# Performance work log

Measured on AMD Instinct MI355X. Metric: run time of the kernel, lower is better.

The kernel has to match this reference:

```python
import jax, jax.numpy as jnp
import numpy as np

NUM_CLUSTERS = 8
DIM_IN, DIM_HID = 1024, 256
N = 65536


def setup_inputs() -> dict:
    key = jax.random.key(0)
    ks = jax.random.split(key, 12)
    s_in = 1.0 / np.sqrt(DIM_IN)
    s_h = 1.0 / np.sqrt(DIM_HID)
    return {
        "x_path": jax.random.normal(ks[0], (1, N, DIM_IN), dtype=jnp.float32),
        "cluster_id": jax.random.randint(ks[1], (N,), 0, NUM_CLUSTERS),
        "W1": jax.random.normal(ks[2], (DIM_HID, DIM_IN), dtype=jnp.float32) * s_in,
        "b1": jax.random.normal(ks[3], (DIM_HID,), dtype=jnp.float32) * s_in,
        "Wf": jax.random.normal(ks[4], (DIM_HID, DIM_HID), dtype=jnp.float32) * s_h,
        "bf": jax.random.normal(ks[5], (DIM_HID,), dtype=jnp.float32) * s_h,
        "Wa": jax.random.normal(ks[6], (DIM_HID, DIM_HID), dtype=jnp.float32) * s_h,
        "ba": jax.random.normal(ks[7], (DIM_HID,), dtype=jnp.float32) * s_h,
        "Wb": jax.random.normal(ks[8], (DIM_HID, DIM_HID), dtype=jnp.float32) * s_h,
        "bb": jax.random.normal(ks[9], (DIM_HID,), dtype=jnp.float32) * s_h,
        "Wc": jax.random.normal(ks[10], (1, DIM_HID), dtype=jnp.float32) * s_h,
        "bc": jax.random.normal(ks[11], (1,), dtype=jnp.float32) * s_h,
    }


def reference(x_path, cluster_id, W1, b1, Wf, bf, Wa, ba, Wb, bb, Wc, bc):
    x = x_path[0]  # [N, dim_in]
    # per-instance 1x1 conv + ReLU (== linear + ReLU)
    h = jax.nn.relu(jnp.einsum('nd,hd->nh', x, W1) + b1)  # [N, dim_hid]
    # segment mean over clusters (AdaptiveAvgPool1d(1) per cluster); empty -> 0
    seg_sum = jax.ops.segment_sum(h, cluster_id, num_segments=NUM_CLUSTERS)
    counts = jax.ops.segment_sum(jnp.ones((h.shape[0],), h.dtype), cluster_id,
                                 num_segments=NUM_CLUSTERS)
    h_cluster = seg_sum / jnp.maximum(counts, 1.0)[:, None]  # [K, dim_hid]
    # attention net: Linear + ReLU (dropout is inference identity)
    h_path = jax.nn.relu(h_cluster @ Wf.T + bf)  # [K, dim_hid]
    # gated attention (CLAM Attn_Net_Gated)
    a = jnp.tanh(h_path @ Wa.T + ba)
    g = jax.nn.sigmoid(h_path @ Wb.T + bb)
    A = (a * g) @ Wc.T + bc            # [K, 1]
    A = jax.nn.softmax(A.T, axis=1)    # [1, K]
    H = A @ h_path                     # [1, dim_hid]
    return H
```

## Files before the change

kernel.cpp:

```cpp
#include <hip/hip_runtime.h>
#include <hip/hip_bf16.h>

#define NN    65536
#define KDIM  1024
#define HDIM  256
#define NC    8
#define BM    64
#define NSP   8

typedef __bf16 bf16x8 __attribute__((ext_vector_type(8)));
typedef float  f32x4  __attribute__((ext_vector_type(4)));
typedef __attribute__((address_space(1))) void GV;
typedef __attribute__((address_space(3))) void LV;

static __device__ __forceinline__ void async_cp16(const void* g, void* l) {
    __builtin_amdgcn_global_load_lds((GV*)g, (LV*)l, 16, 0, 0);
}

#define WAIT_VM16()  __builtin_amdgcn_s_waitcnt(0x4F70)
#define SCHED_PIN()  __builtin_amdgcn_sched_barrier(0)

static __device__ __forceinline__ unsigned short f2bf_rne(float f) {
    unsigned int u = __float_as_uint(f);
    unsigned int r = u + 0x7fffu + ((u >> 16) & 1u);
    return (unsigned short)(r >> 16);
}

static __device__ __forceinline__ unsigned long long pack4bf(float4 v) {
    return (unsigned long long)f2bf_rne(v.x)
         | ((unsigned long long)f2bf_rne(v.y) << 16)
         | ((unsigned long long)f2bf_rne(v.z) << 32)
         | ((unsigned long long)f2bf_rne(v.w) << 48);
}

static __device__ __forceinline__ bf16x8 cvt8(f32x4 a, f32x4 b) {
    __hip_bfloat162 p0 = __float22bfloat162_rn(float2{a[0], a[1]});
    __hip_bfloat162 p1 = __float22bfloat162_rn(float2{a[2], a[3]});
    __hip_bfloat162 p2 = __float22bfloat162_rn(float2{b[0], b[1]});
    __hip_bfloat162 p3 = __float22bfloat162_rn(float2{b[2], b[3]});
    union { __hip_bfloat162 h[4]; bf16x8 v; } u;
    u.h[0] = p0; u.h[1] = p1; u.h[2] = p2; u.h[3] = p3;
    return u.v;
}

__global__ __launch_bounds__(256) void prep_kernel(
    const float* __restrict__ W1, unsigned short* __restrict__ W1b,
    const int* __restrict__ cid, int* __restrict__ cnt_partial)
{
    __shared__ int hcnt[NC];
    if (threadIdx.x < NC) hcnt[threadIdx.x] = 0;
    __syncthreads();

    const int gid  = blockIdx.x * 256 + threadIdx.x;
    const int lane = gid & 63;
    const int j    = (gid >> 6) & 3;
    const int wv   = (gid >> 8) & 3;
    const int kb   = gid >> 10;
    const int n    = wv * 64 + j * 16 + (lane & 15);
    const int k0   = kb * 32 + (lane >> 4) * 8;
    const float* src = W1 + (size_t)n * KDIM + k0;
    float4 v0 = *(const float4*)(src);
    float4 v1 = *(const float4*)(src + 4);
    ulonglong2 pk;
    pk.x = pack4bf(v0);
    pk.y = pack4bf(v1);
    *(ulonglong2*)(W1b + (size_t)gid * 8) = pk;

    atomicAdd(&hcnt[cid[gid]], 1);
    atomicAdd(&hcnt[cid[gid + 32768]], 1);
    __syncthreads();
    if (threadIdx.x < NC)
        cnt_partial[blockIdx.x * NC + threadIdx.x] = hcnt[threadIdx.x];
}

__global__ __launch_bounds__(256, 2) void gemm_kernel(
    const float* __restrict__ x, const int* __restrict__ cid,
    const unsigned short* __restrict__ W1b, const float* __restrict__ b1,
    float* __restrict__ partial)
{
    __shared__ __align__(16) char xs[2 * 32768];
    float* lsums = (float*)xs;
    int*   cids  = (int*)(xs + 8192);

    const int tid  = threadIdx.x;
    const int wave = tid >> 6;
    const int lane = tid & 63;
    const int l15  = lane & 15;
    const int q    = lane >> 4;
    const int row0 = blockIdx.x * BM;
    const int rot  = blockIdx.x & 7;

    int myc = 0;
    if (tid < BM) myc = cid[row0 + tid];

    const int lrow  = lane >> 5;
    const int lslot = lane & 31;

    const int le0 = l15 * 512 + (((2 * q + 0) ^ (l15 & 7)) << 4);
    const int le1 = l15 * 512 + (((2 * q + 1) ^ (l15 & 7)) << 4);

    const unsigned short* bg = W1b + (size_t)(wave * 256 + lane) * 8;

    f32x4 acc[4][4];
    #pragma unroll
    for (int i = 0; i < 4; ++i)
        #pragma unroll
        for (int j = 0; j < 4; ++j)
            #pragma unroll
            for (int r = 0; r < 4; ++r) acc[i][j][r] = 0.0f;

    bf16x8 bA[16], bB[16];

    {
        const int pp0 = rot;
        #pragma unroll
        for (int t = 0; t < 8; ++t) {
            const int r7 = (2 * t + lrow) & 7;
            const float* src = x + (size_t)(row0 + wave * 16 + 2 * t + lrow) * KDIM
                             + pp0 * 128 + ((lslot ^ r7) << 2);
            async_cp16(src, &xs[(wave * 8 + t) * 1024]);
        }
        SCHED_PIN();
        #pragma unroll
        for (int ks = 0; ks < 4; ++ks)
            #pragma unroll
            for (int j = 0; j < 4; ++j)
                bA[ks * 4 + j] = *(const bf16x8*)(bg + (size_t)(pp0 * 4 + ks) * 8192 + j * 512);
        SCHED_PIN();
        WAIT_VM16();
        __builtin_amdgcn_s_barrier();
        SCHED_PIN();
    }

    #pragma unroll
    for (int p = 0; p < NSP; ++p) {
        const int buf = p & 1;
        bf16x8* curB = (p & 1) ? bB : bA;
        bf16x8* nxtB = (p & 1) ? bA : bB;

        if (p + 1 < NSP) {
            const int pp1 = (p + 1 + rot) & 7;
            #pragma unroll
            for (int t = 0; t < 8; ++t) {
                const int r7 = (2 * t + lrow) & 7;
                const float* src = x + (size_t)(row0 + wave * 16 + 2 * t + lrow) * KDIM
                                 + pp1 * 128 + ((lslot ^ r7) << 2);
                async_cp16(src, &xs[(1 - buf) * 32768 + (wave * 8 + t) * 1024]);
            }
            SCHED_PIN();
            #pragma unroll
            for (int ks = 0; ks < 4; ++ks)
                #pragma unroll
                for (int j = 0; j < 4; ++j)
                    nxtB[ks * 4 + j] = *(const bf16x8*)(bg + (size_t)(pp1 * 4 + ks) * 8192 + j * 512);
        }

        #pragma unroll
        for (int ks = 0; ks < 4; ++ks) {
            bf16x8 af[4];
            #pragma unroll
            for (int i = 0; i < 4; ++i) {
                const f32x4 v0 = *(const f32x4*)&xs[buf * 32768 + i * 8192 + ks * 128 + le0];
                const f32x4 v1 = *(const f32x4*)&xs[buf * 32768 + i * 8192 + ks * 128 + le1];
                af[i] = cvt8(v0, v1);
            }
            #pragma unroll
            for (int i = 0; i < 4; ++i)
                #pragma unroll
                for (int j = 0; j < 4; ++j)
                    acc[i][j] = __builtin_amdgcn_mfma_f32_16x16x32_bf16(af[i], curB[ks * 4 + j], acc[i][j], 0, 0, 0);
        }

        if (p + 1 < NSP) {
            SCHED_PIN();
            WAIT_VM16();
            __builtin_amdgcn_s_barrier();
            SCHED_PIN();
        }
    }

    {
        const f32x4 z = {0.0f, 0.0f, 0.0f, 0.0f};
        *(f32x4*)&lsums[tid * 8]     = z;
        *(f32x4*)&lsums[tid * 8 + 4] = z;
        if (tid < BM) cids[tid] = myc;
    }
    __syncthreads();

    float b1v[4];
    #pragma unroll
    for (int j = 0; j < 4; ++j) b1v[j] = b1[wave * 64 + j * 16 + l15];

    #pragma unroll
    for (int i = 0; i < 4; ++i) {
        #pragma unroll
        for (int j = 0; j < 4; ++j) {
            const int col = wave * 64 + j * 16 + l15;
            #pragma unroll
            for (int r = 0; r < 4; ++r) {
                float v = fmaxf(acc[i][j][r] + b1v[j], 0.0f);
                int m = i * 16 + q * 4 + r;
                atomicAdd(&lsums[col * NC + cids[m]], v);
            }
        }
    }
    __syncthreads();
    float* dst = partial + (size_t)blockIdx.x * 2048 + tid * 8;
    *(f32x4*)dst       = *(const f32x4*)&lsums[tid * 8];
    *(f32x4*)(dst + 4) = *(const f32x4*)&lsums[tid * 8 + 4];
}

__global__ __launch_bounds__(256) void reduce_kernel(
    const float* __restrict__ partial, float* __restrict__ stage2)
{
    const int s  = blockIdx.x >> 3;
    const int og = blockIdx.x & 7;
    const int o  = og * 256 + threadIdx.x;
    const float* p = partial + (size_t)s * 128 * 2048 + o;
    float a0=0,a1=0,a2=0,a3=0,a4=0,a5=0,a6=0,a7=0;
    #pragma unroll 4
    for (int pb = 0; pb < 128; pb += 8) {
        a0 += p[(size_t)(pb+0)*2048]; a1 += p[(size_t)(pb+1)*2048];
        a2 += p[(size_t)(pb+2)*2048]; a3 += p[(size_t)(pb+3)*2048];
        a4 += p[(size_t)(pb+4)*2048]; a5 += p[(size_t)(pb+5)*2048];
        a6 += p[(size_t)(pb+6)*2048]; a7 += p[(size_t)(pb+7)*2048];
    }
    stage2[(size_t)s * 2048 + o] = ((a0+a1)+(a2+a3)) + ((a4+a5)+(a6+a7));
}

__global__ __launch_bounds__(256) void head_kernel(
    const float* __restrict__ stage2, const int* __restrict__ cnt_partial,
    const float* __restrict__ Wf, const float* __restrict__ bf1,
    const float* __restrict__ Wa, const float* __restrict__ ba,
    const float* __restrict__ Wb, const float* __restrict__ bb,
    const float* __restrict__ Wc, const float* __restrict__ bc,
    float* __restrict__ out)
{
    __shared__ float hcT[HDIM * NC];
    __shared__ float hpT[HDIM * NC];
    __shared__ float red[NC * 4];
    __shared__ int   cnt_s[256];
    __shared__ float cnt_f[NC];
    const int c = threadIdx.x;
    const int wave = c >> 6, lane = c & 63;

    {
        int k = c & 7, g = c >> 3;
        const int* cp = cnt_partial + g * 32 + k;
        cnt_s[c] = cp[0] + cp[8] + cp[16] + cp[24];
    }
    __syncthreads();
    if (c < NC) {
        int s = 0;
        #pragma unroll
        for (int g = 0; g < 32; ++g) s += cnt_s[g * 8 + c];
        cnt_f[c] = 1.0f / fmaxf((float)s, 1.0f);
    }
    __syncthreads();

    {
        float a[NC] = {0,0,0,0,0,0,0,0};
        #pragma unroll
        for (int s = 0; s < 8; ++s) {
            f32x4 u0 = *(const f32x4*)&stage2[(size_t)s * 2048 + c * 8];
            f32x4 u1 = *(const f32x4*)&stage2[(size_t)s * 2048 + c * 8 + 4];
            a[0]+=u0[0]; a[1]+=u0[1]; a[2]+=u0[2]; a[3]+=u0[3];
            a[4]+=u1[0]; a[5]+=u1[1]; a[6]+=u1[2]; a[7]+=u1[3];
        }
        #pragma unroll
        for (int k = 0; k < NC; ++k) hcT[c * NC + k] = a[k] * cnt_f[k];
    }
    __syncthreads();

    {
        float acc[NC];
        float bias = bf1[c];
        #pragma unroll
        for (int k = 0; k < NC; ++k) acc[k] = bias;
        const float4* wf4 = (const float4*)(Wf + (size_t)c * HDIM);
        for (int d4 = 0; d4 < 64; ++d4) {
            float4 w = wf4[d4];
            #pragma unroll
            for (int e = 0; e < 4; ++e) {
                float wd = (e == 0) ? w.x : (e == 1) ? w.y : (e == 2) ? w.z : w.w;
                const f32x4 h0 = *(const f32x4*)&hcT[(d4 * 4 + e) * NC];
                const f32x4 h1 = *(const f32x4*)&hcT[(d4 * 4 + e) * NC + 4];
                acc[0] += wd * h0[0]; acc[1] += wd * h0[1];
                acc[2] += wd * h0[2]; acc[3] += wd * h0[3];
                acc[4] += wd * h1[0]; acc[5] += wd * h1[1];
                acc[6] += wd * h1[2]; acc[7] += wd * h1[3];
            }
        }
        #pragma unroll
        for (int k = 0; k < NC; ++k) hpT[c * NC + k] = fmaxf(acc[k], 0.0f);
    }
    __syncthreads();

    float za[NC], zb[NC];
    {
        float biasa = ba[c], biasb = bb[c];
        #pragma unroll
        for (int k = 0; k < NC; ++k) { za[k] = biasa; zb[k] = biasb; }
        const float4* wa4 = (const float4*)(Wa + (size_t)c * HDIM);
        const float4* wb4 = (const float4*)(Wb + (size_t)c * HDIM);
        for (int d4 = 0; d4 < 64; ++d4) {
            float4 wa = wa4[d4], wb = wb4[d4];
            #pragma unroll
            for (int e = 0; e < 4; ++e) {
                float wav = (e == 0) ? wa.x : (e == 1) ? wa.y : (e == 2) ? wa.z : wa.w;
                float wbv = (e == 0) ? wb.x : (e == 1) ? wb.y : (e == 2) ? wb.z : wb.w;
                const f32x4 h0 = *(const f32x4*)&hpT[(d4 * 4 + e) * NC];
                const f32x4 h1 = *(const f32x4*)&hpT[(d4 * 4 + e) * NC + 4];
                za[0] += wav * h0[0]; za[1] += wav * h0[1]; za[2] += wav * h0[2]; za[3] += wav * h0[3];
                za[4] += wav * h1[0]; za[5] += wav * h1[1]; za[6] += wav * h1[2]; za[7] += wav * h1[3];
                zb[0] += wbv * h0[0]; zb[1] += wbv * h0[1]; zb[2] += wbv * h0[2]; zb[3] += wbv * h0[3];
                zb[4] += wbv * h1[0]; zb[5] += wbv * h1[1]; zb[6] += wbv * h1[2]; zb[7] += wbv * h1[3];
            }
        }
    }
    float wcv = Wc[c];
    float v[NC];
    #pragma unroll
    for (int k = 0; k < NC; ++k) {
        float a = tanhf(za[k]);
        float g = 1.0f / (1.0f + expf(-zb[k]));
        v[k] = a * g * wcv;
    }
    #pragma unroll
    for (int k = 0; k < NC; ++k) {
        float s = v[k];
        #pragma unroll
        for (int off = 32; off > 0; off >>= 1) s += __shfl_down(s, off, 64);
        if (lane == 0) red[k * 4 + wave] = s;
    }
    __syncthreads();
    float logit[NC], m = -1e30f;
    #pragma unroll
    for (int k = 0; k < NC; ++k) {
        logit[k] = red[k * 4] + red[k * 4 + 1] + red[k * 4 + 2] + red[k * 4 + 3] + bc[0];
        m = fmaxf(m, logit[k]);
    }
    float s = 0.0f, ex[NC];
    #pragma unroll
    for (int k = 0; k < NC; ++k) { ex[k] = expf(logit[k] - m); s += ex[k]; }
    float inv = 1.0f / s;
    float o = 0.0f;
    #pragma unroll
    for (int k = 0; k < NC; ++k) o += ex[k] * inv * hpT[c * NC + k];
    out[c] = o;
}

extern "C" void kernel_launch(void* const* d_in, const int* in_sizes, int n_in,
                              void* d_out, int out_size, void* d_ws, size_t ws_size,
                              hipStream_t stream)
{
    (void)in_sizes; (void)n_in; (void)out_size; (void)ws_size;
    const float* x   = (const float*)d_in[0];
    const int*   cid = (const int*)  d_in[1];
    const float* W1  = (const float*)d_in[2];
    const float* b1  = (const float*)d_in[3];
    const float* Wf  = (const float*)d_in[4];
    const float* bfv = (const float*)d_in[5];
    const float* Wa  = (const float*)d_in[6];
    const float* ba  = (const float*)d_in[7];
    const float* Wb  = (const float*)d_in[8];
    const float* bb  = (const float*)d_in[9];
    const float* Wc  = (const float*)d_in[10];
    const float* bc  = (const float*)d_in[11];
    float* out = (float*)d_out;

    unsigned short* W1b   = (unsigned short*)d_ws;
    int*   cnt_partial    = (int*)  ((char*)d_ws + 524288);
    float* partial        = (float*)((char*)d_ws + 528384);
    float* stage2         = (float*)((char*)d_ws + 528384 + 8388608);

    hipLaunchKernelGGL(prep_kernel,   dim3(128),     dim3(256), 0, stream, W1, W1b, cid, cnt_partial);
    hipLaunchKernelGGL(gemm_kernel,   dim3(NN / BM), dim3(256), 0, stream, x, cid, W1b, b1, partial);
    hipLaunchKernelGGL(reduce_kernel, dim3(64),      dim3(256), 0, stream, partial, stage2);
    hipLaunchKernelGGL(head_kernel,   dim3(1),       dim3(256), 0, stream,
                       stage2, cnt_partial, Wf, bfv, Wa, ba, Wb, bb, Wc, bc, out);
}
```

Measured before the change: 500.1 us.

## Convert x tile to bf16 before staging in LDS, two K-halves

Replaces the double-buffered async global→LDS fp32 pipeline with register loads of x that are converted to bf16 and written to LDS, covering half of K (512) per phase. The MFMA loop then reads bf16 fragments straight from LDS and prefetches B two k-steps ahead. This halves LDS footprint and traffic per element and removes the per-fragment conversion from the inner loop. In exchange, the async copy overlap is lost: each half loads and converts fully before compute, with two barriers per half and no overlap between x loading and MFMA work.

```diff
diff --git a/kernel.cpp b/kernel.cpp
--- a/kernel.cpp
+++ b/kernel.cpp
@@ -6,19 +6,9 @@
 #define HDIM  256
 #define NC    8
 #define BM    64
-#define NSP   8
 
 typedef __bf16 bf16x8 __attribute__((ext_vector_type(8)));
 typedef float  f32x4  __attribute__((ext_vector_type(4)));
-typedef __attribute__((address_space(1))) void GV;
-typedef __attribute__((address_space(3))) void LV;
-
-static __device__ __forceinline__ void async_cp16(const void* g, void* l) {
-    __builtin_amdgcn_global_load_lds((GV*)g, (LV*)l, 16, 0, 0);
-}
-
-#define WAIT_VM16()  __builtin_amdgcn_s_waitcnt(0x4F70)
-#define SCHED_PIN()  __builtin_amdgcn_sched_barrier(0)
 
 static __device__ __forceinline__ unsigned short f2bf_rne(float f) {
     unsigned int u = __float_as_uint(f);
@@ -33,14 +23,12 @@
          | ((unsigned long long)f2bf_rne(v.w) << 48);
 }
 
-static __device__ __forceinline__ bf16x8 cvt8(f32x4 a, f32x4 b) {
-    __hip_bfloat162 p0 = __float22bfloat162_rn(float2{a[0], a[1]});
-    __hip_bfloat162 p1 = __float22bfloat162_rn(float2{a[2], a[3]});
-    __hip_bfloat162 p2 = __float22bfloat162_rn(float2{b[0], b[1]});
-    __hip_bfloat162 p3 = __float22bfloat162_rn(float2{b[2], b[3]});
-    union { __hip_bfloat162 h[4]; bf16x8 v; } u;
-    u.h[0] = p0; u.h[1] = p1; u.h[2] = p2; u.h[3] = p3;
-    return u.v;
+static __device__ __forceinline__ uint2 cvt4_u(float4 v) {
+    union { __hip_bfloat162 h; unsigned int u; } a, b;
+    a.h = __float22bfloat162_rn(float2{v.x, v.y});
+    b.h = __float22bfloat162_rn(float2{v.z, v.w});
+    uint2 r; r.x = a.u; r.y = b.u;
+    return r;
 }
 
 __global__ __launch_bounds__(256) void prep_kernel(
@@ -78,7 +66,7 @@
     const unsigned short* __restrict__ W1b, const float* __restrict__ b1,
     float* __restrict__ partial)
 {
-    __shared__ __align__(16) char xs[2 * 32768];
+    __shared__ __align__(16) char xs[65536];
     float* lsums = (float*)xs;
     int*   cids  = (int*)(xs + 8192);
 
@@ -88,17 +76,10 @@
     const int l15  = lane & 15;
     const int q    = lane >> 4;
     const int row0 = blockIdx.x * BM;
-    const int rot  = blockIdx.x & 7;
 
     int myc = 0;
     if (tid < BM) myc = cid[row0 + tid];
 
-    const int lrow  = lane >> 5;
-    const int lslot = lane & 31;
-
-    const int le0 = l15 * 512 + (((2 * q + 0) ^ (l15 & 7)) << 4);
-    const int le1 = l15 * 512 + (((2 * q + 1) ^ (l15 & 7)) << 4);
-
     const unsigned short* bg = W1b + (size_t)(wave * 256 + lane) * 8;
 
     f32x4 acc[4][4];
@@ -109,74 +90,69 @@
             #pragma unroll
             for (int r = 0; r < 4; ++r) acc[i][j][r] = 0.0f;
 
-    bf16x8 bA[16], bB[16];
-
-    {
-        const int pp0 = rot;
-        #pragma unroll
-        for (int t = 0; t < 8; ++t) {
-            const int r7 = (2 * t + lrow) & 7;
-            const float* src = x + (size_t)(row0 + wave * 16 + 2 * t + lrow) * KDIM
-                             + pp0 * 128 + ((lslot ^ r7) << 2);
-            async_cp16(src, &xs[(wave * 8 + t) * 1024]);
-        }
-        SCHED_PIN();
-        #pragma unroll
-        for (int ks = 0; ks < 4; ++ks)
-            #pragma unroll
-            for (int j = 0; j < 4; ++j)
-                bA[ks * 4 + j] = *(const bf16x8*)(bg + (size_t)(pp0 * 4 + ks) * 8192 + j * 512);
-        SCHED_PIN();
-        WAIT_VM16();
-        __builtin_amdgcn_s_barrier();
-        SCHED_PIN();
-    }
-
-    #pragma unroll
-    for (int p = 0; p < NSP; ++p) {
-        const int buf = p & 1;
-        bf16x8* curB = (p & 1) ? bB : bA;
-        bf16x8* nxtB = (p & 1) ? bA : bB;
-
-        if (p + 1 < NSP) {
-            const int pp1 = (p + 1 + rot) & 7;
+    #pragma unroll
+    for (int kh = 0; kh < 2; ++kh) {
+        {
+            const float* base = x + (size_t)(row0 + wave * 16) * KDIM + kh * 512 + lane * 4;
+            float4 v[2][8];
             #pragma unroll
             for (int t = 0; t < 8; ++t) {
-                const int r7 = (2 * t + lrow) & 7;
-                const float* src = x + (size_t)(row0 + wave * 16 + 2 * t + lrow) * KDIM
-                                 + pp1 * 128 + ((lslot ^ r7) << 2);
-                async_cp16(src, &xs[(1 - buf) * 32768 + (wave * 8 + t) * 1024]);
-            }
-            SCHED_PIN();
-            #pragma unroll
-            for (int ks = 0; ks < 4; ++ks)
+                const int r = t >> 1, c = t & 1;
+                v[0][t] = *(const float4*)(base + (size_t)r * KDIM + c * 256);
+            }
+            #pragma unroll
+            for (int b = 0; b < 4; ++b) {
+                if (b + 1 < 4) {
+                    #pragma unroll
+                    for (int t = 0; t < 8; ++t) {
+                        const int tt = (b + 1) * 8 + t, r = tt >> 1, c = tt & 1;
+                        v[(b + 1) & 1][t] = *(const float4*)(base + (size_t)r * KDIM + c * 256);
+                    }
+                }
                 #pragma unroll
-                for (int j = 0; j < 4; ++j)
-                    nxtB[ks * 4 + j] = *(const bf16x8*)(bg + (size_t)(pp1 * 4 + ks) * 8192 + j * 512);
-        }
-
-        #pragma unroll
-        for (int ks = 0; ks < 4; ++ks) {
-            bf16x8 af[4];
-            #pragma unroll
-            for (int i = 0; i < 4; ++i) {
-                const f32x4 v0 = *(const f32x4*)&xs[buf * 32768 + i * 8192 + ks * 128 + le0];
-                const f32x4 v1 = *(const f32x4*)&xs[buf * 32768 + i * 8192 + ks * 128 + le1];
-                af[i] = cvt8(v0, v1);
-            }
-            #pragma unroll
-            for (int i = 0; i < 4; ++i)
+                for (int t = 0; t < 8; ++t) {
+                    const int tt = b * 8 + t, r = tt >> 1, c = tt & 1;
+                    const int rl = wave * 16 + r;
+                    const int s  = c * 32 + (lane >> 1);
+                    const int h  = lane & 1;
+                    uint2 pk = cvt4_u(v[b & 1][t]);
+                    *(uint2*)&xs[rl * 1024 + (((s ^ (rl & 7)) << 4) | (h << 3))] = pk;
+                }
+            }
+        }
+        __syncthreads();
+
+        {
+            const unsigned short* bgh = bg + (size_t)kh * 16 * 8192;
+            bf16x8 Bf[2][4];
+            #pragma unroll
+            for (int j = 0; j < 4; ++j) Bf[0][j] = *(const bf16x8*)(bgh + j * 512);
+            #pragma unroll
+            for (int j = 0; j < 4; ++j) Bf[1][j] = *(const bf16x8*)(bgh + 8192 + j * 512);
+
+            #pragma unroll
+            for (int kb = 0; kb < 16; ++kb) {
+                const int p = kb & 1;
+                bf16x8 a4[4];
                 #pragma unroll
-                for (int j = 0; j < 4; ++j)
-                    acc[i][j] = __builtin_amdgcn_mfma_f32_16x16x32_bf16(af[i], curB[ks * 4 + j], acc[i][j], 0, 0, 0);
-        }
-
-        if (p + 1 < NSP) {
-            SCHED_PIN();
-            WAIT_VM16();
-            __builtin_amdgcn_s_barrier();
-            SCHED_PIN();
-        }
+                for (int i = 0; i < 4; ++i) {
+                    const int rl = i * 16 + l15;
+                    const int s  = kb * 4 + q;
+                    a4[i] = *(const bf16x8*)&xs[rl * 1024 + ((s ^ (rl & 7)) << 4)];
+                }
+                #pragma unroll
+                for (int i = 0; i < 4; ++i)
+                    #pragma unroll
+                    for (int j = 0; j < 4; ++j)
+                        acc[i][j] = __builtin_amdgcn_mfma_f32_16x16x32_bf16(a4[i], Bf[p][j], acc[i][j], 0, 0, 0);
+                if (kb + 2 < 16) {
+                    #pragma unroll
+                    for (int j = 0; j < 4; ++j)
+                        Bf[p][j] = *(const bf16x8*)(bgh + (size_t)(kb + 2) * 8192 + j * 512);
+                }
+            }
+        }
+        __syncthreads();
     }
 
     {
```

New measurement: 538.5 us. +7.7%, slower.

## Split head into three multi-block kernels, widen reduction, remap GEMM block order

Applied to the files above, without the earlier changes.

The single-block head kernel is split into three kernels: an 8-block Wf layer, an 8-block gated-attention layer writing per-block partial logits, and a one-block softmax/output kernel. The goal is to spread the serial head matmuls over more compute units. The reduce stage is widened from 64 to 128 blocks, each summing 64 partials, and GEMM blocks are remapped with a strided pbid so neighbouring blocks touch different row ranges, which changes the memory access pattern. The cost is two extra kernel launches and round trips through global memory.

```diff
diff --git a/kernel.cpp b/kernel.cpp
--- a/kernel.cpp
+++ b/kernel.cpp
@@ -7,6 +7,7 @@
 #define NC    8
 #define BM    64
 #define NSP   8
+#define RSPL  16
 
 typedef __bf16 bf16x8 __attribute__((ext_vector_type(8)));
 typedef float  f32x4  __attribute__((ext_vector_type(4)));
@@ -87,8 +88,9 @@
     const int lane = tid & 63;
     const int l15  = lane & 15;
     const int q    = lane >> 4;
-    const int row0 = blockIdx.x * BM;
-    const int rot  = blockIdx.x & 7;
+    const int pbid = (blockIdx.x & 7) * 128 + (blockIdx.x >> 3);
+    const int row0 = pbid * BM;
+    const int rot  = (blockIdx.x >> 3) & 7;
 
     int myc = 0;
     if (tid < BM) myc = cid[row0 + tid];
@@ -157,18 +159,18 @@
 
         #pragma unroll
         for (int ks = 0; ks < 4; ++ks) {
-            bf16x8 af[4];
+            bf16x8 a4[4];
             #pragma unroll
             for (int i = 0; i < 4; ++i) {
                 const f32x4 v0 = *(const f32x4*)&xs[buf * 32768 + i * 8192 + ks * 128 + le0];
                 const f32x4 v1 = *(const f32x4*)&xs[buf * 32768 + i * 8192 + ks * 128 + le1];
-                af[i] = cvt8(v0, v1);
+                a4[i] = cvt8(v0, v1);
             }
             #pragma unroll
             for (int i = 0; i < 4; ++i)
                 #pragma unroll
                 for (int j = 0; j < 4; ++j)
-                    acc[i][j] = __builtin_amdgcn_mfma_f32_16x16x32_bf16(af[i], curB[ks * 4 + j], acc[i][j], 0, 0, 0);
+                    acc[i][j] = __builtin_amdgcn_mfma_f32_16x16x32_bf16(a4[i], curB[ks * 4 + j], acc[i][j], 0, 0, 0);
         }
 
         if (p + 1 < NSP) {
@@ -205,7 +207,7 @@
         }
     }
     __syncthreads();
-    float* dst = partial + (size_t)blockIdx.x * 2048 + tid * 8;
+    float* dst = partial + (size_t)pbid * 2048 + tid * 8;
     *(f32x4*)dst       = *(const f32x4*)&lsums[tid * 8];
     *(f32x4*)(dst + 4) = *(const f32x4*)&lsums[tid * 8 + 4];
 }
@@ -216,10 +218,10 @@
     const int s  = blockIdx.x >> 3;
     const int og = blockIdx.x & 7;
     const int o  = og * 256 + threadIdx.x;
-    const float* p = partial + (size_t)s * 128 * 2048 + o;
+    const float* p = partial + (size_t)s * 64 * 2048 + o;
     float a0=0,a1=0,a2=0,a3=0,a4=0,a5=0,a6=0,a7=0;
     #pragma unroll 4
-    for (int pb = 0; pb < 128; pb += 8) {
+    for (int pb = 0; pb < 64; pb += 8) {
         a0 += p[(size_t)(pb+0)*2048]; a1 += p[(size_t)(pb+1)*2048];
         a2 += p[(size_t)(pb+2)*2048]; a3 += p[(size_t)(pb+3)*2048];
         a4 += p[(size_t)(pb+4)*2048]; a5 += p[(size_t)(pb+5)*2048];
@@ -228,125 +230,105 @@
     stage2[(size_t)s * 2048 + o] = ((a0+a1)+(a2+a3)) + ((a4+a5)+(a6+a7));
 }
 
-__global__ __launch_bounds__(256) void head_kernel(
+__global__ __launch_bounds__(256) void headA_kernel(
     const float* __restrict__ stage2, const int* __restrict__ cnt_partial,
     const float* __restrict__ Wf, const float* __restrict__ bf1,
+    float* __restrict__ hp_ws)
+{
+    __shared__ float hcT[HDIM * NC];
+    __shared__ int   cnt_s[256];
+    __shared__ float cnt_f[NC];
+    const int t = threadIdx.x;
+
+    {
+        int k = t & 7, g = t >> 3;
+        const int* cp = cnt_partial + g * 32 + k;
+        cnt_s[t] = cp[0] + cp[8] + cp[16] + cp[24];
+    }
+    __syncthreads();
+    if (t < NC) {
+        int s = 0;
+        #pragma unroll
+        for (int g = 0; g < 32; ++g) s += cnt_s[g * 8 + t];
+        cnt_f[t] = 1.0f / fmaxf((float)s, 1.0f);
+    }
+    __syncthreads();
+
+    {
+        float a[NC] = {0,0,0,0,0,0,0,0};
+        #pragma unroll
+        for (int s = 0; s < RSPL; ++s) {
+            f32x4 u0 = *(const f32x4*)&stage2[(size_t)s * 2048 + t * 8];
+            f32x4 u1 = *(const f32x4*)&stage2[(size_t)s * 2048 + t * 8 + 4];
+            a[0]+=u0[0]; a[1]+=u0[1]; a[2]+=u0[2]; a[3]+=u0[3];
+            a[4]+=u1[0]; a[5]+=u1[1]; a[6]+=u1[2]; a[7]+=u1[3];
+        }
+        #pragma unroll
+        for (int k = 0; k < NC; ++k) hcT[t * NC + k] = a[k] * cnt_f[k];
+    }
+    __syncthreads();
+
+    const int c = blockIdx.x * 32 + (t >> 3);
+    const int k = t & 7;
+    float acc = bf1[c];
+    const float* wf = Wf + (size_t)c * HDIM;
+    for (int d = 0; d < HDIM; ++d)
+        acc += wf[d] * hcT[d * NC + k];
+    hp_ws[k * HDIM + c] = fmaxf(acc, 0.0f);
+}
+
+__global__ __launch_bounds__(256) void headB_kernel(
+    const float* __restrict__ hp_ws,
     const float* __restrict__ Wa, const float* __restrict__ ba,
     const float* __restrict__ Wb, const float* __restrict__ bb,
-    const float* __restrict__ Wc, const float* __restrict__ bc,
-    float* __restrict__ out)
-{
-    __shared__ float hcT[HDIM * NC];
-    __shared__ float hpT[HDIM * NC];
-    __shared__ float red[NC * 4];
-    __shared__ int   cnt_s[256];
-    __shared__ float cnt_f[NC];
+    const float* __restrict__ Wc, float* __restrict__ vpart)
+{
+    __shared__ float vred[256];
+    const int t = threadIdx.x;
+    const int c = blockIdx.x * 32 + (t >> 3);
+    const int k = t & 7;
+    float za = ba[c], zb = bb[c];
+    const float* wa = Wa + (size_t)c * HDIM;
+    const float* wb = Wb + (size_t)c * HDIM;
+    const float* hp = hp_ws + (size_t)k * HDIM;
+    for (int d = 0; d < HDIM; ++d) {
+        float h = hp[d];
+        za += wa[d] * h;
+        zb += wb[d] * h;
+    }
+    float a = tanhf(za);
+    float g = 1.0f / (1.0f + expf(-zb));
+    vred[t] = a * g * Wc[c];
+    __syncthreads();
+    if (t < NC) {
+        float s = 0.0f;
+        #pragma unroll
+        for (int cl = 0; cl < 32; ++cl) s += vred[cl * 8 + t];
+        vpart[blockIdx.x * NC + t] = s;
+    }
+}
+
+__global__ __launch_bounds__(256) void headC_kernel(
+    const float* __restrict__ hp_ws, const float* __restrict__ vpart,
+    const float* __restrict__ bc, float* __restrict__ out)
+{
     const int c = threadIdx.x;
-    const int wave = c >> 6, lane = c & 63;
-
-    {
-        int k = c & 7, g = c >> 3;
-        const int* cp = cnt_partial + g * 32 + k;
-        cnt_s[c] = cp[0] + cp[8] + cp[16] + cp[24];
-    }
-    __syncthreads();
-    if (c < NC) {
-        int s = 0;
-        #pragma unroll
-        for (int g = 0; g < 32; ++g) s += cnt_s[g * 8 + c];
-        cnt_f[c] = 1.0f / fmaxf((float)s, 1.0f);
-    }
-    __syncthreads();
-
-    {
-        float a[NC] = {0,0,0,0,0,0,0,0};
-        #pragma unroll
-        for (int s = 0; s < 8; ++s) {
-            f32x4 u0 = *(const f32x4*)&stage2[(size_t)s * 2048 + c * 8];
-            f32x4 u1 = *(const f32x4*)&stage2[(size_t)s * 2048 + c * 8 + 4];
-            a[0]+=u0[0]; a[1]+=u0[1]; a[2]+=u0[2]; a[3]+=u0[3];
-            a[4]+=u1[0]; a[5]+=u1[1]; a[6]+=u1[2]; a[7]+=u1[3];
-        }
-        #pragma unroll
-        for (int k = 0; k < NC; ++k) hcT[c * NC + k] = a[k] * cnt_f[k];
-    }
-    __syncthreads();
-
-    {
-        float acc[NC];
-        float bias = bf1[c];
-        #pragma unroll
-        for (int k = 0; k < NC; ++k) acc[k] = bias;
-        const float4* wf4 = (const float4*)(Wf + (size_t)c * HDIM);
-        for (int d4 = 0; d4 < 64; ++d4) {
-            float4 w = wf4[d4];
-            #pragma unroll
-            for (int e = 0; e < 4; ++e) {
-                float wd = (e == 0) ? w.x : (e == 1) ? w.y : (e == 2) ? w.z : w.w;
-                const f32x4 h0 = *(const f32x4*)&hcT[(d4 * 4 + e) * NC];
-                const f32x4 h1 = *(const f32x4*)&hcT[(d4 * 4 + e) * NC + 4];
-                acc[0] += wd * h0[0]; acc[1] += wd * h0[1];
-                acc[2] += wd * h0[2]; acc[3] += wd * h0[3];
-                acc[4] += wd * h1[0]; acc[5] += wd * h1[1];
-                acc[6] += wd * h1[2]; acc[7] += wd * h1[3];
-            }
-        }
-        #pragma unroll
-        for (int k = 0; k < NC; ++k) hpT[c * NC + k] = fmaxf(acc[k], 0.0f);
-    }
-    __syncthreads();
-
-    float za[NC], zb[NC];
-    {
-        float biasa = ba[c], biasb = bb[c];
-        #pragma unroll
-        for (int k = 0; k < NC; ++k) { za[k] = biasa; zb[k] = biasb; }
-        const float4* wa4 = (const float4*)(Wa + (size_t)c * HDIM);
-        const float4* wb4 = (const float4*)(Wb + (size_t)c * HDIM);
-        for (int d4 = 0; d4 < 64; ++d4) {
-            float4 wa = wa4[d4], wb = wb4[d4];
-            #pragma unroll
-            for (int e = 0; e < 4; ++e) {
-                float wav = (e == 0) ? wa.x : (e == 1) ? wa.y : (e == 2) ? wa.z : wa.w;
-                float wbv = (e == 0) ? wb.x : (e == 1) ? wb.y : (e == 2) ? wb.z : wb.w;
-                const f32x4 h0 = *(const f32x4*)&hpT[(d4 * 4 + e) * NC];
-                const f32x4 h1 = *(const f32x4*)&hpT[(d4 * 4 + e) * NC + 4];
-                za[0] += wav * h0[0]; za[1] += wav * h0[1]; za[2] += wav * h0[2]; za[3] += wav * h0[3];
-                za[4] += wav * h1[0]; za[5] += wav * h1[1]; za[6] += wav * h1[2]; za[7] += wav * h1[3];
-                zb[0] += wbv * h0[0]; zb[1] += wbv * h0[1]; zb[2] += wbv * h0[2]; zb[3] += wbv * h0[3];
-                zb[4] += wbv * h1[0]; zb[5] += wbv * h1[1]; zb[6] += wbv * h1[2]; zb[7] += wbv * h1[3];
-            }
-        }
-    }
-    float wcv = Wc[c];
-    float v[NC];
+    float logit[NC], m = -1e30f;
     #pragma unroll
     for (int k = 0; k < NC; ++k) {
-        float a = tanhf(za[k]);
-        float g = 1.0f / (1.0f + expf(-zb[k]));
-        v[k] = a * g * wcv;
-    }
-    #pragma unroll
-    for (int k = 0; k < NC; ++k) {
-        float s = v[k];
-        #pragma unroll
-        for (int off = 32; off > 0; off >>= 1) s += __shfl_down(s, off, 64);
-        if (lane == 0) red[k * 4 + wave] = s;
-    }
-    __syncthreads();
-    float logit[NC], m = -1e30f;
-    #pragma unroll
-    for (int k = 0; k < NC; ++k) {
-        logit[k] = red[k * 4] + red[k * 4 + 1] + red[k * 4 + 2] + red[k * 4 + 3] + bc[0];
-        m = fmaxf(m, logit[k]);
-    }
-    float s = 0.0f, ex[NC];
-    #pragma unroll
-    for (int k = 0; k < NC; ++k) { ex[k] = expf(logit[k] - m); s += ex[k]; }
-    float inv = 1.0f / s;
+        float s = bc[0];
+        #pragma unroll
+        for (int b = 0; b < 8; ++b) s += vpart[b * NC + k];
+        logit[k] = s;
+        m = fmaxf(m, s);
+    }
+    float sum = 0.0f, ex[NC];
+    #pragma unroll
+    for (int k = 0; k < NC; ++k) { ex[k] = expf(logit[k] - m); sum += ex[k]; }
+    float inv = 1.0f / sum;
     float o = 0.0f;
     #pragma unroll
-    for (int k = 0; k < NC; ++k) o += ex[k] * inv * hpT[c * NC + k];
+    for (int k = 0; k < NC; ++k) o += ex[k] * inv * hp_ws[k * HDIM + c];
     out[c] = o;
 }
 
@@ -372,11 +354,14 @@
     unsigned short* W1b   = (unsigned short*)d_ws;
     int*   cnt_partial    = (int*)  ((char*)d_ws + 524288);
     float* partial        = (float*)((char*)d_ws + 528384);
-    float* stage2         = (float*)((char*)d_ws + 528384 + 8388608);
+    float* stage2         = (float*)((char*)d_ws + 8916992);
+    float* hp_ws          = (float*)((char*)d_ws + 9048064);
+    float* vpart          = (float*)((char*)d_ws + 9056256);
 
     hipLaunchKernelGGL(prep_kernel,   dim3(128),     dim3(256), 0, stream, W1, W1b, cid, cnt_partial);
     hipLaunchKernelGGL(gemm_kernel,   dim3(NN / BM), dim3(256), 0, stream, x, cid, W1b, b1, partial);
-    hipLaunchKernelGGL(reduce_kernel, dim3(64),      dim3(256), 0, stream, partial, stage2);
-    hipLaunchKernelGGL(head_kernel,   dim3(1),       dim3(256), 0, stream,
-                       stage2, cnt_partial, Wf, bfv, Wa, ba, Wb, bb, Wc, bc, out);
-}
+    hipLaunchKernelGGL(reduce_kernel, dim3(128),     dim3(256), 0, stream, partial, stage2);
+    hipLaunchKernelGGL(headA_kernel,  dim3(8),       dim3(256), 0, stream, stage2, cnt_partial, Wf, bfv, hp_ws);
+    hipLaunchKernelGGL(headB_kernel,  dim3(8),       dim3(256), 0, stream, hp_ws, Wa, ba, Wb, bb, Wc, vpart);
+    hipLaunchKernelGGL(headC_kernel,  dim3(1),       dim3(256), 0, stream, hp_ws, vpart, bc, out);
+}
```

Result: faster. 476.4 us (-4.7%).
